# Kernel tuning notes

Hardware: AMD Instinct MI355X
Metric: run time of the kernel (lower is better)

The kernel has to match this reference:

```python
import jax, jax.numpy as jnp
import numpy as np

B, N, XDIM, EDIM, H = 4, 256, 256, 128, 8
DF = XDIM // H


def _linear_params(key, din, dout):
    k1, k2 = jax.random.split(key)
    s = 1.0 / np.sqrt(din)
    W = jax.random.uniform(k1, (din, dout), minval=-s, maxval=s, dtype=jnp.float32)
    b = jax.random.uniform(k2, (dout,), minval=-s, maxval=s, dtype=jnp.float32)
    return W, b


def setup_inputs() -> dict:
    key = jax.random.key(0)
    ks = jax.random.split(key, 9)
    x = jax.random.normal(ks[0], (B, N, XDIM), dtype=jnp.float32)
    e = jax.random.normal(ks[1], (B, N, N, EDIM), dtype=jnp.float32)
    Wq, bq = _linear_params(ks[2], XDIM, XDIM)
    Wk, bk = _linear_params(ks[3], XDIM, XDIM)
    Wv, bv = _linear_params(ks[4], XDIM, XDIM)
    Wem, bem = _linear_params(ks[5], EDIM, XDIM)  # e_mul
    Wea, bea = _linear_params(ks[6], EDIM, XDIM)  # e_add
    Wxo, bxo = _linear_params(ks[7], XDIM, XDIM)  # x_out
    Weo, beo = _linear_params(ks[8], XDIM, EDIM)  # e_out
    return {"x": x, "e": e, "Wq": Wq, "bq": bq, "Wk": Wk, "bk": bk,
            "Wv": Wv, "bv": bv, "Wem": Wem, "bem": bem, "Wea": Wea, "bea": bea,
            "Wxo": Wxo, "bxo": bxo, "Weo": Weo, "beo": beo}


def reference(x, e, Wq, bq, Wk, bk, Wv, bv, Wem, bem, Wea, bea, Wxo, bxo, Weo, beo):
    Bq, Nq, _ = x.shape
    # per-node projections -> [B, N, H, DF]
    Q = (x @ Wq + bq).reshape(Bq, Nq, H, DF)
    K = (x @ Wk + bk).reshape(Bq, Nq, H, DF)
    V = (x @ Wv + bv).reshape(Bq, Nq, H, DF)
    # broadcasted outer product: Y[b,i,j,h,d] = Q[b,i,h,d] * K[b,j,h,d] / sqrt(DF)
    Y = Q[:, :, None] * K[:, None] * (1.0 / np.sqrt(DF))  # [B,N,N,H,DF]
    # edge modulation
    E1 = (e @ Wem + bem).reshape(Bq, Nq, Nq, H, DF)
    E2 = (e @ Wea + bea).reshape(Bq, Nq, Nq, H, DF)
    Y = Y * (E1 + 1.0) + E2
    # new edge features
    newE = Y.reshape(Bq, Nq, Nq, XDIM) @ Weo + beo  # [B,N,N,EDIM]
    # attention: softmax over the FIRST node axis (dim=1), as in the torch code
    attn = jax.nn.softmax(Y, axis=1)  # [B,N,N,H,DF]
    # weighted_V[b,j,h,d] = sum_i attn[b,i,j,h,d] * V[b,j,h,d]
    weighted_V = jnp.sum(attn * V[:, None], axis=1)  # [B,N,H,DF]
    newX = weighted_V.reshape(Bq, Nq, XDIM) @ Wxo + bxo  # [B,N,XDIM]
    return (newX, newE)
```

## Files before the change

kernel.cpp:

```cpp
#include <hip/hip_runtime.h>

#define NN 256
#define XD 256
#define ED 128

typedef __attribute__((ext_vector_type(8))) short short8;
typedef __attribute__((ext_vector_type(4))) float f32x4;

__device__ __forceinline__ unsigned short f2bf(float f) {
    unsigned u = __builtin_bit_cast(unsigned, f);
    u += 0x7FFF + ((u >> 16) & 1);
    return (unsigned short)(u >> 16);
}

#define MFMA16(a, b, c) __builtin_amdgcn_mfma_f32_16x16x32_bf16(a, b, c, 0, 0, 0)

__global__ __launch_bounds__(256) void wprep_kernel(
    const float* __restrict__ Wq, const float* __restrict__ Wk,
    const float* __restrict__ Wv, const float* __restrict__ Wxo,
    const float* __restrict__ Wem, const float* __restrict__ Wea,
    const float* __restrict__ Weo,
    short* __restrict__ WqT, short* __restrict__ WkT,
    short* __restrict__ WvT, short* __restrict__ WxoT,
    short* __restrict__ WemT, short* __restrict__ WeaT,
    short* __restrict__ WeoT)
{
    __shared__ float sT[32][33];
    int blk = blockIdx.x;
    const float* src; short* dst; int din, dout, tile;
    if (blk < 256) {
        int m = blk >> 6; tile = blk & 63; din = 256; dout = 256;
        src = m == 0 ? Wq : (m == 1 ? Wk : (m == 2 ? Wv : Wxo));
        dst = m == 0 ? WqT : (m == 1 ? WkT : (m == 2 ? WvT : WxoT));
    } else if (blk < 320) {
        int m = (blk - 256) >> 5; tile = (blk - 256) & 31; din = 128; dout = 256;
        src = m == 0 ? Wem : Wea; dst = m == 0 ? WemT : WeaT;
    } else {
        tile = blk - 320; din = 256; dout = 128;
        src = Weo; dst = WeoT;
    }
    int ksh = (din == 256) ? 3 : 2;
    int kt = tile & ((1 << ksh) - 1);
    int nt = tile >> ksh;
    int c = threadIdx.x & 31, rbase = threadIdx.x >> 5;
    #pragma unroll
    for (int p = 0; p < 4; ++p) {
        int r = rbase + p * 8;
        sT[r][c] = src[(kt * 32 + r) * dout + nt * 32 + c];
    }
    __syncthreads();
    #pragma unroll
    for (int p = 0; p < 4; ++p) {
        int r = rbase + p * 8;
        dst[(nt * 32 + r) * din + kt * 32 + c] = (short)f2bf(sT[c][r]);
    }
}

__global__ __launch_bounds__(512) void proj_qk_kernel(
    const float* __restrict__ x, const short* __restrict__ WqT,
    const short* __restrict__ WkT, const float* __restrict__ bq,
    const float* __restrict__ bk, float* __restrict__ Qs,
    float* __restrict__ KT)
{
    __shared__ unsigned short sX[64 * 264];
    const int blk = blockIdx.x;
    const int mtile = blk >> 1;
    const int mat   = blk & 1;
    const int tid = threadIdx.x, wave = tid >> 6, lane = tid & 63;
    const int quad = lane >> 4, l16 = lane & 15;

    {
        const float4* src4 = (const float4*)(x + (size_t)mtile * 64 * XD);
        #pragma unroll
        for (int it = 0; it < 8; ++it) {
            int idx4 = tid + it * 512;
            float4 v = src4[idx4];
            int elem = idx4 * 4, row = elem >> 8, col = elem & 255;
            short4 p = make_short4((short)f2bf(v.x), (short)f2bf(v.y),
                                   (short)f2bf(v.z), (short)f2bf(v.w));
            *(short4*)&sX[row * 264 + col] = p;
        }
    }
    __syncthreads();

    const short* WT   = mat ? WkT : WqT;
    const float* bias = mat ? bk : bq;
    const int c0 = wave * 32;

    f32x4 acc[4][2] = {};
    for (int ks = 0; ks < 8; ++ks) {
        short8 bfrag[2];
        #pragma unroll
        for (int ct = 0; ct < 2; ++ct)
            bfrag[ct] = *(const short8*)&WT[(c0 + ct * 16 + l16) * 256 + ks * 32 + quad * 8];
        #pragma unroll
        for (int mt = 0; mt < 4; ++mt) {
            short8 a = *(const short8*)&sX[(mt * 16 + l16) * 264 + ks * 32 + quad * 8];
            acc[mt][0] = MFMA16(a, bfrag[0], acc[mt][0]);
            acc[mt][1] = MFMA16(a, bfrag[1], acc[mt][1]);
        }
    }

    if (mat == 0) {
        #pragma unroll
        for (int mt = 0; mt < 4; ++mt)
            #pragma unroll
            for (int ct = 0; ct < 2; ++ct) {
                int cc = c0 + ct * 16 + l16;
                float bb = bias[cc];
                #pragma unroll
                for (int r = 0; r < 4; ++r)
                    Qs[(size_t)(mtile * 64 + mt * 16 + quad * 4 + r) * 256 + cc] =
                        (acc[mt][ct][r] + bb) * 0.17677669529663687f;
            }
    } else {
        int b = mtile >> 2, j0p = (mtile & 3) * 64;
        #pragma unroll
        for (int mt = 0; mt < 4; ++mt)
            #pragma unroll
            for (int ct = 0; ct < 2; ++ct) {
                int cc = c0 + ct * 16 + l16;
                float bb = bias[cc];
                f32x4 st;
                #pragma unroll
                for (int r = 0; r < 4; ++r) st[r] = acc[mt][ct][r] + bb;
                *(f32x4*)&KT[(size_t)(b * 256 + cc) * 256 + j0p + mt * 16 + quad * 4] = st;
            }
    }
}

__global__ __launch_bounds__(512) void proj_vx_kernel(
    const float* __restrict__ x, const short* __restrict__ WvT,
    const float* __restrict__ bv, const short* __restrict__ WxoT,
    const float* __restrict__ bxo, float* __restrict__ outX)
{
    __shared__ unsigned short sX[64 * 264];
    __shared__ unsigned short sV[64 * 264];
    const int mtile = blockIdx.x;
    const int tid = threadIdx.x, wave = tid >> 6, lane = tid & 63;
    const int quad = lane >> 4, l16 = lane & 15;

    {
        const float4* src4 = (const float4*)(x + (size_t)mtile * 64 * XD);
        #pragma unroll
        for (int it = 0; it < 8; ++it) {
            int idx4 = tid + it * 512;
            float4 v = src4[idx4];
            int elem = idx4 * 4, row = elem >> 8, col = elem & 255;
            short4 p = make_short4((short)f2bf(v.x), (short)f2bf(v.y),
                                   (short)f2bf(v.z), (short)f2bf(v.w));
            *(short4*)&sX[row * 264 + col] = p;
        }
    }
    __syncthreads();

    const int c0 = wave * 32;
    f32x4 acc[4][2] = {};
    for (int ks = 0; ks < 8; ++ks) {
        short8 bfrag[2];
        #pragma unroll
        for (int ct = 0; ct < 2; ++ct)
            bfrag[ct] = *(const short8*)&WvT[(c0 + ct * 16 + l16) * 256 + ks * 32 + quad * 8];
        #pragma unroll
        for (int mt = 0; mt < 4; ++mt) {
            short8 a = *(const short8*)&sX[(mt * 16 + l16) * 264 + ks * 32 + quad * 8];
            acc[mt][0] = MFMA16(a, bfrag[0], acc[mt][0]);
            acc[mt][1] = MFMA16(a, bfrag[1], acc[mt][1]);
        }
    }
    #pragma unroll
    for (int mt = 0; mt < 4; ++mt)
        #pragma unroll
        for (int ct = 0; ct < 2; ++ct) {
            int cc = c0 + ct * 16 + l16;
            float bb = bv[cc];
            #pragma unroll
            for (int r = 0; r < 4; ++r)
                sV[(mt * 16 + quad * 4 + r) * 264 + cc] = f2bf(acc[mt][ct][r] + bb);
        }
    __syncthreads();

    f32x4 acc2[4][2] = {};
    for (int ks = 0; ks < 8; ++ks) {
        short8 bfrag[2];
        #pragma unroll
        for (int ct = 0; ct < 2; ++ct)
            bfrag[ct] = *(const short8*)&WxoT[(c0 + ct * 16 + l16) * 256 + ks * 32 + quad * 8];
        #pragma unroll
        for (int mt = 0; mt < 4; ++mt) {
            short8 a = *(const short8*)&sV[(mt * 16 + l16) * 264 + ks * 32 + quad * 8];
            acc2[mt][0] = MFMA16(a, bfrag[0], acc2[mt][0]);
            acc2[mt][1] = MFMA16(a, bfrag[1], acc2[mt][1]);
        }
    }
    #pragma unroll
    for (int mt = 0; mt < 4; ++mt)
        #pragma unroll
        for (int ct = 0; ct < 2; ++ct) {
            int cc = c0 + ct * 16 + l16;
            float bb = bxo[cc];
            #pragma unroll
            for (int r = 0; r < 4; ++r)
                outX[(size_t)(mtile * 64 + mt * 16 + quad * 4 + r) * 256 + cc] =
                    acc2[mt][ct][r] + bb;
        }
}

__global__ __launch_bounds__(256, 3) void fused_edge_kernel(
    const float* __restrict__ e, const float* __restrict__ Qs,
    const float* __restrict__ KT, const short* __restrict__ WemT,
    const short* __restrict__ WeaT, const short* __restrict__ WeoT,
    const float* __restrict__ bem, const float* __restrict__ bea,
    const float* __restrict__ beo, float* __restrict__ outE)
{
    __shared__ unsigned short sE[64 * 140];
    __shared__ unsigned short sY[64 * 268];

    const int blk  = blockIdx.x;
    const int jq   = blk & 3;
    const int i    = (blk >> 2) & 255;
    const int b    = blk >> 10;
    const int j0   = jq * 64;
    const int tid  = threadIdx.x;
    const int wave = tid >> 6;
    const int lane = tid & 63;
    const int quad = lane >> 4;
    const int l16  = lane & 15;

    {
        const float4* src4 = (const float4*)(e + (size_t)((b * NN + i) * NN + j0) * ED);
        #pragma unroll
        for (int it = 0; it < 8; ++it) {
            int idx4 = tid + it * 256;
            float4 v = src4[idx4];
            int elem = idx4 * 4, row = elem >> 7, col = elem & 127;
            short4 p = make_short4((short)f2bf(v.x), (short)f2bf(v.y),
                                   (short)f2bf(v.z), (short)f2bf(v.w));
            *(short4*)&sE[row * 140 + col] = p;
        }
    }

    const float* Qrow = Qs + (size_t)(b * NN + i) * XD;
    float bo[2];
    #pragma unroll
    for (int ct = 0; ct < 2; ++ct) bo[ct] = beo[wave * 32 + ct * 16 + l16];

    __syncthreads();

    #pragma unroll
    for (int p = 0; p < 2; ++p) {
        const int c0 = wave * 32 + p * 128;
        float qsv[2], bmv[2], bav[2];
        int ktA[2];
        #pragma unroll
        for (int ct = 0; ct < 2; ++ct) {
            int cc = c0 + ct * 16 + l16;
            qsv[ct] = Qrow[cc];
            bmv[ct] = bem[cc] + 1.0f;
            bav[ct] = bea[cc];
            ktA[ct] = (b * 256 + cc) * 256 + j0 + quad * 4;
        }
        short8 B1[4][2], B2[4][2];
        #pragma unroll
        for (int ks = 0; ks < 4; ++ks)
            #pragma unroll
            for (int ct = 0; ct < 2; ++ct) {
                int n = c0 + ct * 16 + l16;
                B1[ks][ct] = *(const short8*)&WemT[n * 128 + ks * 32 + quad * 8];
                B2[ks][ct] = *(const short8*)&WeaT[n * 128 + ks * 32 + quad * 8];
            }
        #pragma unroll
        for (int mc = 0; mc < 4; ++mc) {
            const int m0 = mc * 16;
            f32x4 aE1[2] = {}, aE2[2] = {};
            #pragma unroll
            for (int ks = 0; ks < 4; ++ks) {
                short8 a = *(const short8*)&sE[(m0 + l16) * 140 + ks * 32 + quad * 8];
                aE1[0] = MFMA16(a, B1[ks][0], aE1[0]);
                aE1[1] = MFMA16(a, B1[ks][1], aE1[1]);
                aE2[0] = MFMA16(a, B2[ks][0], aE2[0]);
                aE2[1] = MFMA16(a, B2[ks][1], aE2[1]);
            }
            #pragma unroll
            for (int ct = 0; ct < 2; ++ct) {
                f32x4 kv = *(const f32x4*)&KT[ktA[ct] + m0];
                int cc = c0 + ct * 16 + l16;
                #pragma unroll
                for (int r = 0; r < 4; ++r) {
                    float y = qsv[ct] * kv[r] * (aE1[ct][r] + bmv[ct])
                              + (aE2[ct][r] + bav[ct]);
                    sY[(m0 + quad * 4 + r) * 268 + cc] = f2bf(y);
                }
            }
        }
    }
    __syncthreads();

    short8 B3[8][2];
    #pragma unroll
    for (int ks = 0; ks < 8; ++ks)
        #pragma unroll
        for (int ct = 0; ct < 2; ++ct)
            B3[ks][ct] = *(const short8*)&WeoT[(wave * 32 + ct * 16 + l16) * 256 + ks * 32 + quad * 8];
    f32x4 acc2[4][2] = {};
    #pragma unroll
    for (int ks = 0; ks < 8; ++ks) {
        #pragma unroll
        for (int mt = 0; mt < 4; ++mt) {
            short8 a = *(const short8*)&sY[(mt * 16 + l16) * 268 + ks * 32 + quad * 8];
            acc2[mt][0] = MFMA16(a, B3[ks][0], acc2[mt][0]);
            acc2[mt][1] = MFMA16(a, B3[ks][1], acc2[mt][1]);
        }
    }
    float* outBase = outE + (size_t)((b * NN + i) * NN + j0) * ED;
    #pragma unroll
    for (int mt = 0; mt < 4; ++mt)
        #pragma unroll
        for (int ct = 0; ct < 2; ++ct) {
            int col = wave * 32 + ct * 16 + l16;
            #pragma unroll
            for (int r = 0; r < 4; ++r)
                outBase[(size_t)(mt * 16 + quad * 4 + r) * ED + col] = acc2[mt][ct][r] + bo[ct];
        }
}

extern "C" void kernel_launch(void* const* d_in, const int* in_sizes, int n_in,
                              void* d_out, int out_size, void* d_ws, size_t ws_size,
                              hipStream_t stream)
{
    const float* x   = (const float*)d_in[0];
    const float* e   = (const float*)d_in[1];
    const float* Wq  = (const float*)d_in[2];
    const float* bq  = (const float*)d_in[3];
    const float* Wk  = (const float*)d_in[4];
    const float* bk  = (const float*)d_in[5];
    const float* Wv  = (const float*)d_in[6];
    const float* bv  = (const float*)d_in[7];
    const float* Wem = (const float*)d_in[8];
    const float* bem = (const float*)d_in[9];
    const float* Wea = (const float*)d_in[10];
    const float* bea = (const float*)d_in[11];
    const float* Wxo = (const float*)d_in[12];
    const float* bxo = (const float*)d_in[13];
    const float* Weo = (const float*)d_in[14];
    const float* beo = (const float*)d_in[15];

    float* outX = (float*)d_out;
    float* outE = (float*)d_out + 262144;

    float* Qs   = (float*)d_ws;
    float* KT   = Qs + 262144;
    short* WqT  = (short*)(KT + 262144);
    short* WkT  = WqT + 65536;
    short* WvT  = WkT + 65536;
    short* WxoT = WvT + 65536;
    short* WemT = WxoT + 65536;
    short* WeaT = WemT + 32768;
    short* WeoT = WeaT + 32768;

    hipLaunchKernelGGL(wprep_kernel, dim3(352), dim3(256), 0, stream,
                       Wq, Wk, Wv, Wxo, Wem, Wea, Weo,
                       WqT, WkT, WvT, WxoT, WemT, WeaT, WeoT);
    hipLaunchKernelGGL(proj_qk_kernel, dim3(32), dim3(512), 0, stream,
                       x, WqT, WkT, bq, bk, Qs, KT);
    hipLaunchKernelGGL(proj_vx_kernel, dim3(16), dim3(512), 0, stream,
                       x, WvT, bv, WxoT, bxo, outX);
    hipLaunchKernelGGL(fused_edge_kernel, dim3(4096), dim3(256), 0, stream,
                       e, Qs, KT, WemT, WeaT, WeoT, bem, bea, beo, outE);
}
```

Measured before the change: 366.3 us.

## Transpose edge MFMA roles, halve edge tile, and swizzle shared memory

The fused edge kernel now uses 32-row j tiles (8192 blocks) and swaps MFMA operand roles, so weights become the A operand and edge rows the B operand. Accumulators then hold 4 consecutive channels per lane, which allows vectorized loads of Q, K, biases and float4 output stores. K is stored row-major instead of transposed. Shared memory uses XOR swizzling instead of padding, and the launch bound is raised to 4 blocks per SM. The intent is more occupancy, fewer bank conflicts and coalesced stores. The cost is that weight fragments are reloaded per block with less reuse per tile.

```diff
diff --git a/kernel.cpp b/kernel.cpp
--- a/kernel.cpp
+++ b/kernel.cpp
@@ -60,7 +60,7 @@
     const float* __restrict__ x, const short* __restrict__ WqT,
     const short* __restrict__ WkT, const float* __restrict__ bq,
     const float* __restrict__ bk, float* __restrict__ Qs,
-    float* __restrict__ KT)
+    float* __restrict__ Ks)
 {
     __shared__ unsigned short sX[64 * 264];
     const int blk = blockIdx.x;
@@ -85,6 +85,8 @@
 
     const short* WT   = mat ? WkT : WqT;
     const float* bias = mat ? bk : bq;
+    const float scale = mat ? 1.0f : 0.17677669529663687f;
+    float* out        = mat ? Ks : Qs;
     const int c0 = wave * 32;
 
     f32x4 acc[4][2] = {};
@@ -100,33 +102,17 @@
             acc[mt][1] = MFMA16(a, bfrag[1], acc[mt][1]);
         }
     }
-
-    if (mat == 0) {
-        #pragma unroll
-        for (int mt = 0; mt < 4; ++mt)
+    #pragma unroll
+    for (int mt = 0; mt < 4; ++mt)
+        #pragma unroll
+        for (int ct = 0; ct < 2; ++ct) {
+            int cc = c0 + ct * 16 + l16;
+            float bb = bias[cc];
             #pragma unroll
-            for (int ct = 0; ct < 2; ++ct) {
-                int cc = c0 + ct * 16 + l16;
-                float bb = bias[cc];
-                #pragma unroll
-                for (int r = 0; r < 4; ++r)
-                    Qs[(size_t)(mtile * 64 + mt * 16 + quad * 4 + r) * 256 + cc] =
-                        (acc[mt][ct][r] + bb) * 0.17677669529663687f;
-            }
-    } else {
-        int b = mtile >> 2, j0p = (mtile & 3) * 64;
-        #pragma unroll
-        for (int mt = 0; mt < 4; ++mt)
-            #pragma unroll
-            for (int ct = 0; ct < 2; ++ct) {
-                int cc = c0 + ct * 16 + l16;
-                float bb = bias[cc];
-                f32x4 st;
-                #pragma unroll
-                for (int r = 0; r < 4; ++r) st[r] = acc[mt][ct][r] + bb;
-                *(f32x4*)&KT[(size_t)(b * 256 + cc) * 256 + j0p + mt * 16 + quad * 4] = st;
-            }
-    }
+            for (int r = 0; r < 4; ++r)
+                out[(size_t)(mtile * 64 + mt * 16 + quad * 4 + r) * 256 + cc] =
+                    (acc[mt][ct][r] + bb) * scale;
+        }
 }
 
 __global__ __launch_bounds__(512) void proj_vx_kernel(
@@ -206,21 +192,21 @@
         }
 }
 
-__global__ __launch_bounds__(256, 3) void fused_edge_kernel(
+__global__ __launch_bounds__(256, 4) void fused_edge_kernel(
     const float* __restrict__ e, const float* __restrict__ Qs,
-    const float* __restrict__ KT, const short* __restrict__ WemT,
+    const float* __restrict__ Ks, const short* __restrict__ WemT,
     const short* __restrict__ WeaT, const short* __restrict__ WeoT,
     const float* __restrict__ bem, const float* __restrict__ bea,
     const float* __restrict__ beo, float* __restrict__ outE)
 {
-    __shared__ unsigned short sE[64 * 140];
-    __shared__ unsigned short sY[64 * 268];
+    __shared__ __align__(16) unsigned short sE[32 * 128];
+    __shared__ __align__(16) unsigned short sY[32 * 256];
 
     const int blk  = blockIdx.x;
-    const int jq   = blk & 3;
-    const int i    = (blk >> 2) & 255;
-    const int b    = blk >> 10;
-    const int j0   = jq * 64;
+    const int jq   = blk & 7;
+    const int i    = (blk >> 3) & 255;
+    const int b    = blk >> 11;
+    const int j0   = jq * 32;
     const int tid  = threadIdx.x;
     const int wave = tid >> 6;
     const int lane = tid & 63;
@@ -230,98 +216,88 @@
     {
         const float4* src4 = (const float4*)(e + (size_t)((b * NN + i) * NN + j0) * ED);
         #pragma unroll
-        for (int it = 0; it < 8; ++it) {
+        for (int it = 0; it < 4; ++it) {
             int idx4 = tid + it * 256;
             float4 v = src4[idx4];
-            int elem = idx4 * 4, row = elem >> 7, col = elem & 127;
+            int row = idx4 >> 5;
+            int colb = (idx4 & 31) * 8;
             short4 p = make_short4((short)f2bf(v.x), (short)f2bf(v.y),
                                    (short)f2bf(v.z), (short)f2bf(v.w));
-            *(short4*)&sE[row * 140 + col] = p;
-        }
-    }
+            *(short4*)((char*)sE + (row * 256 + (colb ^ ((row & 7) << 4)))) = p;
+        }
+    }
+    __syncthreads();
 
     const float* Qrow = Qs + (size_t)(b * NN + i) * XD;
-    float bo[2];
-    #pragma unroll
-    for (int ct = 0; ct < 2; ++ct) bo[ct] = beo[wave * 32 + ct * 16 + l16];
-
-    __syncthreads();
-
-    #pragma unroll
-    for (int p = 0; p < 2; ++p) {
-        const int c0 = wave * 32 + p * 128;
-        float qsv[2], bmv[2], bav[2];
-        int ktA[2];
-        #pragma unroll
-        for (int ct = 0; ct < 2; ++ct) {
-            int cc = c0 + ct * 16 + l16;
-            qsv[ct] = Qrow[cc];
-            bmv[ct] = bem[cc] + 1.0f;
-            bav[ct] = bea[cc];
-            ktA[ct] = (b * 256 + cc) * 256 + j0 + quad * 4;
-        }
-        short8 B1[4][2], B2[4][2];
-        #pragma unroll
-        for (int ks = 0; ks < 4; ++ks)
+    const int cW = wave * 64;
+
+    #pragma unroll
+    for (int cT = 0; cT < 4; ++cT) {
+        const int c0 = cW + cT * 16;
+        const int cq = c0 + quad * 4;
+        f32x4 q4  = *(const f32x4*)&Qrow[cq];
+        f32x4 bm4 = *(const f32x4*)&bem[cq];
+        bm4 = bm4 + 1.0f;
+        f32x4 ba4 = *(const f32x4*)&bea[cq];
+        f32x4 k4[2];
+        #pragma unroll
+        for (int jT = 0; jT < 2; ++jT)
+            k4[jT] = *(const f32x4*)&Ks[(size_t)(b * NN + j0 + jT * 16 + l16) * XD + cq];
+
+        f32x4 a1[2] = {}, a2[2] = {};
+        #pragma unroll
+        for (int ks = 0; ks < 4; ++ks) {
+            short8 A1 = *(const short8*)&WemT[(c0 + l16) * 128 + ks * 32 + quad * 8];
+            short8 A2 = *(const short8*)&WeaT[(c0 + l16) * 128 + ks * 32 + quad * 8];
             #pragma unroll
-            for (int ct = 0; ct < 2; ++ct) {
-                int n = c0 + ct * 16 + l16;
-                B1[ks][ct] = *(const short8*)&WemT[n * 128 + ks * 32 + quad * 8];
-                B2[ks][ct] = *(const short8*)&WeaT[n * 128 + ks * 32 + quad * 8];
+            for (int jT = 0; jT < 2; ++jT) {
+                int jr = jT * 16 + l16;
+                short8 Bf = *(const short8*)((const char*)sE +
+                             (jr * 256 + ((ks * 64 + quad * 16) ^ ((jr & 7) << 4))));
+                a1[jT] = MFMA16(A1, Bf, a1[jT]);
+                a2[jT] = MFMA16(A2, Bf, a2[jT]);
             }
-        #pragma unroll
-        for (int mc = 0; mc < 4; ++mc) {
-            const int m0 = mc * 16;
-            f32x4 aE1[2] = {}, aE2[2] = {};
-            #pragma unroll
-            for (int ks = 0; ks < 4; ++ks) {
-                short8 a = *(const short8*)&sE[(m0 + l16) * 140 + ks * 32 + quad * 8];
-                aE1[0] = MFMA16(a, B1[ks][0], aE1[0]);
-                aE1[1] = MFMA16(a, B1[ks][1], aE1[1]);
-                aE2[0] = MFMA16(a, B2[ks][0], aE2[0]);
-                aE2[1] = MFMA16(a, B2[ks][1], aE2[1]);
-            }
-            #pragma unroll
-            for (int ct = 0; ct < 2; ++ct) {
-                f32x4 kv = *(const f32x4*)&KT[ktA[ct] + m0];
-                int cc = c0 + ct * 16 + l16;
-                #pragma unroll
-                for (int r = 0; r < 4; ++r) {
-                    float y = qsv[ct] * kv[r] * (aE1[ct][r] + bmv[ct])
-                              + (aE2[ct][r] + bav[ct]);
-                    sY[(m0 + quad * 4 + r) * 268 + cc] = f2bf(y);
-                }
-            }
-        }
-    }
-    __syncthreads();
-
-    short8 B3[8][2];
-    #pragma unroll
-    for (int ks = 0; ks < 8; ++ks)
-        #pragma unroll
-        for (int ct = 0; ct < 2; ++ct)
-            B3[ks][ct] = *(const short8*)&WeoT[(wave * 32 + ct * 16 + l16) * 256 + ks * 32 + quad * 8];
-    f32x4 acc2[4][2] = {};
+        }
+        #pragma unroll
+        for (int jT = 0; jT < 2; ++jT) {
+            int jr = jT * 16 + l16;
+            f32x4 y = q4 * k4[jT] * (a1[jT] + bm4) + (a2[jT] + ba4);
+            short4 yp = make_short4((short)f2bf(y[0]), (short)f2bf(y[1]),
+                                    (short)f2bf(y[2]), (short)f2bf(y[3]));
+            *(short4*)((char*)sY + (jr * 512 + ((cq * 2) ^ ((jr & 7) << 4)))) = yp;
+        }
+    }
+    __syncthreads();
+
+    const int oW = wave * 32;
+    f32x4 acc[2][2] = {};
     #pragma unroll
     for (int ks = 0; ks < 8; ++ks) {
-        #pragma unroll
-        for (int mt = 0; mt < 4; ++mt) {
-            short8 a = *(const short8*)&sY[(mt * 16 + l16) * 268 + ks * 32 + quad * 8];
-            acc2[mt][0] = MFMA16(a, B3[ks][0], acc2[mt][0]);
-            acc2[mt][1] = MFMA16(a, B3[ks][1], acc2[mt][1]);
+        short8 A[2];
+        #pragma unroll
+        for (int oT = 0; oT < 2; ++oT)
+            A[oT] = *(const short8*)&WeoT[(oW + oT * 16 + l16) * 256 + ks * 32 + quad * 8];
+        #pragma unroll
+        for (int jT = 0; jT < 2; ++jT) {
+            int jr = jT * 16 + l16;
+            short8 Bf = *(const short8*)((const char*)sY +
+                         (jr * 512 + ((ks * 64 + quad * 16) ^ ((jr & 7) << 4))));
+            acc[0][jT] = MFMA16(A[0], Bf, acc[0][jT]);
+            acc[1][jT] = MFMA16(A[1], Bf, acc[1][jT]);
         }
     }
     float* outBase = outE + (size_t)((b * NN + i) * NN + j0) * ED;
     #pragma unroll
-    for (int mt = 0; mt < 4; ++mt)
-        #pragma unroll
-        for (int ct = 0; ct < 2; ++ct) {
-            int col = wave * 32 + ct * 16 + l16;
-            #pragma unroll
-            for (int r = 0; r < 4; ++r)
-                outBase[(size_t)(mt * 16 + quad * 4 + r) * ED + col] = acc2[mt][ct][r] + bo[ct];
-        }
+    for (int oT = 0; oT < 2; ++oT) {
+        int oq = oW + oT * 16 + quad * 4;
+        f32x4 bo4 = *(const f32x4*)&beo[oq];
+        #pragma unroll
+        for (int jT = 0; jT < 2; ++jT) {
+            int jr = jT * 16 + l16;
+            f32x4 st = acc[oT][jT] + bo4;
+            *(f32x4*)&outBase[(size_t)jr * ED + oq] = st;
+        }
+    }
 }
 
 extern "C" void kernel_launch(void* const* d_in, const int* in_sizes, int n_in,
@@ -349,8 +325,8 @@
     float* outE = (float*)d_out + 262144;
 
     float* Qs   = (float*)d_ws;
-    float* KT   = Qs + 262144;
-    short* WqT  = (short*)(KT + 262144);
+    float* Ks   = Qs + 262144;
+    short* WqT  = (short*)(Ks + 262144);
     short* WkT  = WqT + 65536;
     short* WvT  = WkT + 65536;
     short* WxoT = WvT + 65536;
@@ -362,9 +338,9 @@
                        Wq, Wk, Wv, Wxo, Wem, Wea, Weo,
                        WqT, WkT, WvT, WxoT, WemT, WeaT, WeoT);
     hipLaunchKernelGGL(proj_qk_kernel, dim3(32), dim3(512), 0, stream,
-                       x, WqT, WkT, bq, bk, Qs, KT);
+                       x, WqT, WkT, bq, bk, Qs, Ks);
     hipLaunchKernelGGL(proj_vx_kernel, dim3(16), dim3(512), 0, stream,
                        x, WvT, bv, WxoT, bxo, outX);
-    hipLaunchKernelGGL(fused_edge_kernel, dim3(4096), dim3(256), 0, stream,
-                       e, Qs, KT, WemT, WeaT, WeoT, bem, bea, beo, outE);
-}
+    hipLaunchKernelGGL(fused_edge_kernel, dim3(8192), dim3(256), 0, stream,
+                       e, Qs, Ks, WemT, WeaT, WeoT, bem, bea, beo, outE);
+}
```

Result: slower. 469.0 us (+28.0%).
